# Performance work log

Hardware: AMD Instinct MI355X
Metric: run time of the kernel (lower is better)

The kernel has to match this reference:

```python
import jax, jax.numpy as jnp
import numpy as np

N = 4000000
MAX_TRI = 6  # 16 coords -> 8 vertices -> at most 6 fan triangles


def setup_inputs() -> dict:
    key = jax.random.key(0)
    k1, k2 = jax.random.split(key)
    int_pts = jax.random.normal(k1, (N, 16), dtype=jnp.float32)
    num_of_inter = jax.random.randint(k2, (N,), 0, 9, dtype=jnp.int32)
    return {"int_pts": int_pts, "num_of_inter": num_of_inter}


def reference(int_pts, num_of_inter):
    # Fan triangulation from vertex 0: tri_i = (p0, p_{i+1}, p_{i+2}), i in [0, num-3]
    pts = int_pts.reshape(-1, 8, 2)            # [N, 8, 2]
    p1 = pts[:, 0:1, :]                        # [N, 1, 2] (apex, broadcast)
    p2 = pts[:, 1:7, :]                        # [N, 6, 2]
    p3 = pts[:, 2:8, :]                        # [N, 6, 2]
    cross = (p1[..., 0] - p3[..., 0]) * (p2[..., 1] - p3[..., 1]) \
          - (p1[..., 1] - p3[..., 1]) * (p2[..., 0] - p3[..., 0])  # [N, 6]
    tri_area = jnp.abs(cross) * 0.5
    mask = jnp.arange(MAX_TRI, dtype=jnp.int32)[None, :] < (num_of_inter[:, None] - 2)
    return jnp.sum(jnp.where(mask, tri_area, 0.0), axis=1)  # [N]
```

## Files before the change

### kernel.cpp

```cpp
#include <hip/hip_runtime.h>

#define N_ROWS 4000000
#define MAX_TRI 6

__global__ __launch_bounds__(256) void rinter_area_kernel(
    const float* __restrict__ int_pts,
    const int* __restrict__ num_of_inter,
    float* __restrict__ out,
    int n)
{
    int i = blockIdx.x * blockDim.x + threadIdx.x;
    if (i >= n) return;

    const float4* p = (const float4*)(int_pts + (size_t)i * 16);
    float4 v0 = p[0];
    float4 v1 = p[1];
    float4 v2 = p[2];
    float4 v3 = p[3];

    float pts[16];
    pts[0]=v0.x; pts[1]=v0.y; pts[2]=v0.z; pts[3]=v0.w;
    pts[4]=v1.x; pts[5]=v1.y; pts[6]=v1.z; pts[7]=v1.w;
    pts[8]=v2.x; pts[9]=v2.y; pts[10]=v2.z; pts[11]=v2.w;
    pts[12]=v3.x; pts[13]=v3.y; pts[14]=v3.z; pts[15]=v3.w;

    float p1x = pts[0];
    float p1y = pts[1];

    int nt = num_of_inter[i] - 2;

    float acc = 0.0f;
    #pragma unroll
    for (int j = 0; j < MAX_TRI; ++j) {
        float p2x = pts[2 * (1 + j)];
        float p2y = pts[2 * (1 + j) + 1];
        float p3x = pts[2 * (2 + j)];
        float p3y = pts[2 * (2 + j) + 1];
        float cross = (p1x - p3x) * (p2y - p3y) - (p1y - p3y) * (p2x - p3x);
        float area = fabsf(cross) * 0.5f;
        acc += (j < nt) ? area : 0.0f;
    }
    out[i] = acc;
}

extern "C" void kernel_launch(void* const* d_in, const int* in_sizes, int n_in,
                              void* d_out, int out_size, void* d_ws, size_t ws_size,
                              hipStream_t stream) {
    const float* int_pts      = (const float*)d_in[0];
    const int*   num_of_inter = (const int*)d_in[1];
    float*       out          = (float*)d_out;
    int n = in_sizes[1];

    const int block = 256;
    const int grid = (n + block - 1) / block;
    rinter_area_kernel<<<grid, block, 0, stream>>>(int_pts, num_of_inter, out, n);
}
```

Measured before the change: 348.2 us.

## Split each row across four lanes, skip empty rows, use grid-stride loop

Each row is now handled by four lanes that each load one float4, so a wavefront's loads are contiguous and coalesced instead of strided by 64 bytes per thread. Shuffles share the apex and the neighbouring vertex between lanes, and a quad reduction sums the partial areas. Rows with fewer than three vertices skip the point load entirely, which cuts memory traffic for about a third of the rows. A persistent grid-stride loop with a prefetched count replaces the one-thread-per-row launch.

```diff
diff --git a/kernel.cpp b/kernel.cpp
--- a/kernel.cpp
+++ b/kernel.cpp
@@ -1,57 +1,58 @@
 #include <hip/hip_runtime.h>
 
-#define N_ROWS 4000000
-#define MAX_TRI 6
-
 __global__ __launch_bounds__(256) void rinter_area_kernel(
-    const float* __restrict__ int_pts,
+    const float4* __restrict__ pts4,
     const int* __restrict__ num_of_inter,
     float* __restrict__ out,
     int n)
 {
-    int i = blockIdx.x * blockDim.x + threadIdx.x;
-    if (i >= n) return;
+    const int q = threadIdx.x & 3;
+    const int gpb = blockDim.x >> 2;
+    const int gstride = gridDim.x * gpb;
+    int row = blockIdx.x * gpb + (threadIdx.x >> 2);
 
-    const float4* p = (const float4*)(int_pts + (size_t)i * 16);
-    float4 v0 = p[0];
-    float4 v1 = p[1];
-    float4 v2 = p[2];
-    float4 v3 = p[3];
+    int nv = (row < n) ? num_of_inter[row] : 2;
 
-    float pts[16];
-    pts[0]=v0.x; pts[1]=v0.y; pts[2]=v0.z; pts[3]=v0.w;
-    pts[4]=v1.x; pts[5]=v1.y; pts[6]=v1.z; pts[7]=v1.w;
-    pts[8]=v2.x; pts[9]=v2.y; pts[10]=v2.z; pts[11]=v2.w;
-    pts[12]=v3.x; pts[13]=v3.y; pts[14]=v3.z; pts[15]=v3.w;
+    while (row < n) {
+        int nrow = row + gstride;
+        int nnv = (nrow < n) ? num_of_inter[nrow] : 2;
 
-    float p1x = pts[0];
-    float p1y = pts[1];
+        int nt = nv - 2;
+        float acc = 0.0f;
+        if (nt > 0) {
+            float4 a = pts4[(size_t)row * 4 + q];
 
-    int nt = num_of_inter[i] - 2;
+            float p1x = __shfl(a.x, 0, 4);
+            float p1y = __shfl(a.y, 0, 4);
+            float nx2 = __shfl_down(a.x, 1, 4);
+            float ny2 = __shfl_down(a.y, 1, 4);
 
-    float acc = 0.0f;
-    #pragma unroll
-    for (int j = 0; j < MAX_TRI; ++j) {
-        float p2x = pts[2 * (1 + j)];
-        float p2y = pts[2 * (1 + j) + 1];
-        float p3x = pts[2 * (2 + j)];
-        float p3y = pts[2 * (2 + j) + 1];
-        float cross = (p1x - p3x) * (p2y - p3y) - (p1y - p3y) * (p2x - p3x);
-        float area = fabsf(cross) * 0.5f;
-        acc += (j < nt) ? area : 0.0f;
+            float crossA = (p1x - a.z) * (a.y - a.w) - (p1y - a.w) * (a.x - a.z);
+            float crossB = (p1x - nx2) * (a.w - ny2) - (p1y - ny2) * (a.z - nx2);
+
+            acc  = (nt > 2 * q - 1) ? fabsf(crossA) * 0.5f : 0.0f;
+            acc += (nt > 2 * q)     ? fabsf(crossB) * 0.5f : 0.0f;
+
+            acc += __shfl_xor(acc, 1, 4);
+            acc += __shfl_xor(acc, 2, 4);
+        }
+        if (q == 0) out[row] = acc;
+
+        row = nrow;
+        nv = nnv;
     }
-    out[i] = acc;
 }
 
 extern "C" void kernel_launch(void* const* d_in, const int* in_sizes, int n_in,
                               void* d_out, int out_size, void* d_ws, size_t ws_size,
                               hipStream_t stream) {
-    const float* int_pts      = (const float*)d_in[0];
-    const int*   num_of_inter = (const int*)d_in[1];
-    float*       out          = (float*)d_out;
+    const float4* pts4          = (const float4*)d_in[0];
+    const int*    num_of_inter  = (const int*)d_in[1];
+    float*        out           = (float*)d_out;
     int n = in_sizes[1];
 
     const int block = 256;
-    const int grid = (n + block - 1) / block;
-    rinter_area_kernel<<<grid, block, 0, stream>>>(int_pts, num_of_inter, out, n);
+    int blocks_needed = (n + 63) / 64;
+    int grid = blocks_needed < 2048 ? blocks_needed : 2048;
+    rinter_area_kernel<<<grid, block, 0, stream>>>(pts4, num_of_inter, out, n);
 }
```

Result: no change. 347.1 us (-0.3%).
